# Kernel tuning notes

Measured on AMD Instinct MI355X. Metric: run time of the kernel, lower is better.

Reference implementation:

```python
import jax, jax.numpy as jnp
import numpy as np
from jax import lax

B, NBB, C, H, W = 32, 16, 1024, 22, 22
P = 3            # pooled output size (3x3)
SCALE = 1.0 / 16.0
EPS = 1e-5


def setup_inputs() -> dict:
    key = jax.random.key(0)
    ks = jax.random.split(key, 12)
    feat = jax.random.normal(ks[0], (B, C, H, W), jnp.float32)
    # bbox in xywh image coords, in-range for a 352x352 search region
    xy = jax.random.uniform(ks[1], (B, NBB, 2), jnp.float32, 0.0, 250.0)
    wh = jax.random.uniform(ks[2], (B, NBB, 2), jnp.float32, 16.0, 100.0)
    bbox = jnp.concatenate([xy, wh], axis=-1)
    conv_w = jax.random.normal(ks[3], (C, C, 3, 3), jnp.float32) * 0.01
    conv_b = jnp.zeros((C,), jnp.float32)
    bn_gamma = jnp.ones((C,), jnp.float32)
    bn_beta = jnp.zeros((C,), jnp.float32)
    bn_mean = jax.random.normal(ks[4], (C,), jnp.float32) * 0.1
    bn_var = jax.random.uniform(ks[5], (C,), jnp.float32, 0.5, 1.5)
    w1 = jax.random.normal(ks[6], (C // 2, C), jnp.float32) * 0.02
    b1 = jnp.zeros((C // 2,), jnp.float32)
    w2 = jax.random.normal(ks[7], (C // 2, C // 2), jnp.float32) * 0.02
    b2 = jnp.zeros((C // 2,), jnp.float32)
    w3 = jax.random.normal(ks[8], (512, C // 2), jnp.float32) * 0.02
    b3 = jnp.zeros((512,), jnp.float32)
    return dict(feat=feat, bbox=bbox, conv_w=conv_w, conv_b=conv_b,
                bn_gamma=bn_gamma, bn_beta=bn_beta, bn_mean=bn_mean, bn_var=bn_var,
                w1=w1, b1=b1, w2=w2, b2=b2, w3=w3, b3=b3)


def _hat_int(t):
    # Antiderivative of the bilinear hat h(u)=max(0,1-|u|), clipped to support.
    t = jnp.clip(t, -1.0, 1.0)
    return t + 0.5 - 0.5 * t * jnp.abs(t)


def _bin_weights(lo, bw, n):
    # lo, bw: [B, NBB].  Returns exact integral weights [B, NBB, P, n]:
    # W[b,r,p,i] = integral over bin p of hat(x - i) dx  (PrRoI closed form).
    p = jnp.arange(P, dtype=lo.dtype)
    xs = lo[..., None] + p * bw[..., None]          # [B,NBB,P] bin starts
    xe = xs + bw[..., None]                          # bin ends
    i = jnp.arange(n, dtype=lo.dtype)
    return _hat_int(xe[..., None] - i) - _hat_int(xs[..., None] - i)


def reference(feat, bbox, conv_w, conv_b, bn_gamma, bn_beta, bn_mean, bn_var,
              w1, b1, w2, b2, w3, b3):
    # --- PrRoI pooling (exact separable bilinear integral) ---
    x1 = bbox[..., 0] * SCALE
    y1 = bbox[..., 1] * SCALE
    x2 = (bbox[..., 0] + bbox[..., 2]) * SCALE
    y2 = (bbox[..., 1] + bbox[..., 3]) * SCALE
    bw = (x2 - x1) / P
    bh = (y2 - y1) / P
    Wx = _bin_weights(x1, bw, W)                     # [B,NBB,P,W]
    Wy = _bin_weights(y1, bh, H)                     # [B,NBB,P,H]
    pooled = jnp.einsum('bchw,bnqh,bnpw->bncqp', feat, Wy, Wx)  # [B,NBB,C,P,P]
    area = jnp.maximum(bw * bh, 0.0)[..., None, None, None]
    pooled = jnp.where(area > 0, pooled / jnp.maximum(area, 1e-12), 0.0)
    x = pooled.reshape(B * NBB, C, P, P)

    # --- conv_bn_relu: 3x3 conv, valid padding -> 1x1, BN (eval), ReLU ---
    x = lax.conv_general_dilated(x, conv_w, (1, 1), 'VALID',
                                 dimension_numbers=('NCHW', 'OIHW', 'NCHW'))
    x = x + conv_b[:, None, None]
    x = (x - bn_mean[:, None, None]) * (bn_gamma * lax.rsqrt(bn_var + EPS))[:, None, None]
    x = x + bn_beta[:, None, None]
    x = jax.nn.relu(x)

    # --- MLP head ---
    x = x.reshape(B * NBB, C)
    x = jax.nn.relu(x @ w1.T + b1)
    x = jax.nn.relu(x @ w2.T + b2)
    x = x @ w3.T + b3
    return x.reshape(B, NBB, 512)
```

## Files before the change

### kernel.cpp

```cpp
#include <hip/hip_runtime.h>
#include <hip/hip_bf16.h>

#define B_    32
#define NBB_  16
#define C_    1024
#define NROI  512
#define KCONV 9216
#define SCALE_ (1.0f/16.0f)
#define EPS_  1e-5f

using f32x4  = __attribute__((ext_vector_type(4))) float;
using bf16x8 = __attribute__((ext_vector_type(8))) short;

__device__ __forceinline__ unsigned f2bf(float f) {
  union { float f; unsigned u; } x; x.f = f;
  unsigned r = x.u + 0x7fffu + ((x.u >> 16) & 1u);
  return r >> 16;
}

__device__ __forceinline__ unsigned pk_bf16(float lo, float hi) {
  __hip_bfloat162 h = __float22bfloat162_rn(make_float2(lo, hi));
  return *reinterpret_cast<unsigned*>(&h);
}

__device__ __forceinline__ float hat_int(float t) {
  t = fminf(fmaxf(t, -1.f), 1.f);
  return t + 0.5f - 0.5f * t * fabsf(t);
}

__device__ __forceinline__ void glds16(const void* g, void* l) {
  __builtin_amdgcn_global_load_lds((const __attribute__((address_space(1))) void*)g,
                                   (__attribute__((address_space(3))) void*)l, 16, 0, 0);
}

__global__ __launch_bounds__(256) void prep_all(
    const float* __restrict__ bbox, const float* __restrict__ conv_w,
    const float* __restrict__ w1, const float* __restrict__ w2, const float* __restrict__ w3,
    unsigned short* __restrict__ W2d, unsigned short* __restrict__ Wfb,
    unsigned short* __restrict__ o1, unsigned short* __restrict__ o2,
    unsigned short* __restrict__ o3)
{
  __shared__ __align__(16) char psm[18504];
  int tid = threadIdx.x;
  int bx = blockIdx.x;

  if (bx < 32) {
    int b = bx;
    float* wyS = (float*)psm;
    float* wxS = wyS + 1056;
    for (int t = tid; t < 352; t += 256) {
      int n = t / 22, i = t - n * 22;
      float4 bb = ((const float4*)bbox)[b*16 + n];
      float x1 = bb.x * SCALE_, y1 = bb.y * SCALE_;
      float x2 = (bb.x + bb.z) * SCALE_, y2 = (bb.y + bb.w) * SCALE_;
      float bw = (x2 - x1) / 3.f, bh = (y2 - y1) / 3.f;
      float area = fmaxf(bw * bh, 0.f);
      float inv = area > 0.f ? 1.f / fmaxf(area, 1e-12f) : 0.f;
      float fi = (float)i;
#pragma unroll
      for (int q = 0; q < 3; ++q) {
        float sy = y1 + q * bh;
        wyS[n*66 + q*22 + i] = hat_int(sy + bh - fi) - hat_int(sy - fi);
        float sx = x1 + q * bw;
        wxS[n*66 + q*22 + i] = (hat_int(sx + bw - fi) - hat_int(sx - fi)) * inv;
      }
    }
    __syncthreads();
    if (tid < 144) {
      int n = tid / 9, qp = tid - n*9, q = qp / 3, p = qp - q*3;
      const float* wyp = wyS + n*66 + q*22;
      const float* wxp = wxS + n*66 + p*22;
      unsigned short* out = W2d + ((size_t)b*144 + tid) * 512;
      for (int h = 0; h < 22; ++h) {
        float yv = wyp[h];
        int kb = h * 22;
#pragma unroll
        for (int w = 0; w < 22; w += 2)
          *(unsigned*)&out[kb + w] = pk_bf16(yv * wxp[w], yv * wxp[w+1]);
      }
#pragma unroll
      for (int k = 484; k < 512; k += 2) *(unsigned*)&out[k] = 0u;
    }
  } else if (bx < 1056) {
    int o = bx - 32;
    unsigned short (*T)[1028] = (unsigned short(*)[1028])psm;
    const float4* src = (const float4*)(conv_w + (size_t)o * 9216);
#pragma unroll
    for (int it = 0; it < 9; ++it) {
      int i = tid + it * 256;
      float4 v = src[i];
      int e = i * 4;
      { int c = e / 9,     qp = e - c*9;             T[qp][c] = (unsigned short)f2bf(v.x); }
      { int ee = e+1; int c = ee / 9, qp = ee - c*9; T[qp][c] = (unsigned short)f2bf(v.y); }
      { int ee = e+2; int c = ee / 9, qp = ee - c*9; T[qp][c] = (unsigned short)f2bf(v.z); }
      { int ee = e+3; int c = ee / 9, qp = ee - c*9; T[qp][c] = (unsigned short)f2bf(v.w); }
    }
    __syncthreads();
    unsigned short* dst = Wfb + (size_t)o * 9216;
#pragma unroll
    for (int qp = 0; qp < 9; ++qp) {
      uint2 w = *(const uint2*)&T[qp][tid * 4];
      ((uint2*)(dst + qp * 1024))[tid] = w;
    }
  } else {
    int i = (bx - 1056) * 256 + tid;
    const float* src; unsigned short* dst; int g;
    if (i < 65536)      { src = w1; dst = o1; g = i; }
    else if (i < 98304) { src = w2; dst = o2; g = i - 65536; }
    else                { src = w3; dst = o3; g = i - 98304; }
    float4 a = ((const float4*)src)[2*g];
    float4 b = ((const float4*)src)[2*g + 1];
    uint4 pk;
    pk.x = pk_bf16(a.x, a.y); pk.y = pk_bf16(a.z, a.w);
    pk.z = pk_bf16(b.x, b.y); pk.w = pk_bf16(b.z, b.w);
    ((uint4*)dst)[g] = pk;
  }
}

__global__ __launch_bounds__(384) void pool_gemm(const float* __restrict__ feat,
                                                 const unsigned short* __restrict__ W2d,
                                                 unsigned short* __restrict__ X) {
  __shared__ __align__(16) unsigned short Bs[64 * 72];
  int tid = threadIdx.x;
  int nch = blockIdx.x, b = blockIdx.y;
  int lane = tid & 63, wid = tid >> 6;
  int wm = wid >> 1, wn = wid & 1;
  int l15 = lane & 15, kg = lane >> 4;
  const unsigned short* w2b = W2d + (size_t)b * 144 * 512;
  const float* fb = feat + ((size_t)b * C_ + (size_t)nch * 64) * 484;
  f32x4 acc[3][2] = {};

  int c0 = tid >> 4,        f40 = tid & 15;
  int i1 = tid + 384;  int c1 = i1 >> 4, f41 = i1 & 15;
  int i2 = tid + 768;  bool has2 = i2 < 1024; int c2 = i2 >> 4, f42 = i2 & 15;
  float4 bR0, bR1, bR2;

#define LOADB(s) do { \
    bR0 = (((s) < 7 || f40 <= 8) ? *(const float4*)(fb + (size_t)c0*484 + (s)*64 + f40*4) : make_float4(0,0,0,0)); \
    bR1 = (((s) < 7 || f41 <= 8) ? *(const float4*)(fb + (size_t)c1*484 + (s)*64 + f41*4) : make_float4(0,0,0,0)); \
    if (has2) bR2 = (((s) < 7 || f42 <= 8) ? *(const float4*)(fb + (size_t)c2*484 + (s)*64 + f42*4) : make_float4(0,0,0,0)); \
  } while (0)

  LOADB(0);
#pragma unroll
  for (int s = 0; s < 8; ++s) {
    __syncthreads();
    {
      uint2 p0; p0.x = pk_bf16(bR0.x, bR0.y); p0.y = pk_bf16(bR0.z, bR0.w);
      *(uint2*)&Bs[c0*72 + f40*4] = p0;
      uint2 p1; p1.x = pk_bf16(bR1.x, bR1.y); p1.y = pk_bf16(bR1.z, bR1.w);
      *(uint2*)&Bs[c1*72 + f41*4] = p1;
      if (has2) {
        uint2 p2; p2.x = pk_bf16(bR2.x, bR2.y); p2.y = pk_bf16(bR2.z, bR2.w);
        *(uint2*)&Bs[c2*72 + f42*4] = p2;
      }
    }
    if (s < 7) LOADB(s + 1);
    __syncthreads();

    bf16x8 af[3][2], bf[2][2];
#pragma unroll
    for (int fm = 0; fm < 3; ++fm)
#pragma unroll
      for (int kk = 0; kk < 2; ++kk)
        af[fm][kk] = *(const bf16x8*)(w2b + (size_t)(wm*48 + fm*16 + l15) * 512 + s*64 + kk*32 + kg*8);
#pragma unroll
    for (int fn = 0; fn < 2; ++fn)
#pragma unroll
      for (int kk = 0; kk < 2; ++kk)
        bf[fn][kk] = *(const bf16x8*)&Bs[(wn*32 + fn*16 + l15) * 72 + kk*32 + kg*8];
#pragma unroll
    for (int fm = 0; fm < 3; ++fm)
#pragma unroll
      for (int fn = 0; fn < 2; ++fn) {
        acc[fm][fn] = __builtin_amdgcn_mfma_f32_16x16x32_bf16(af[fm][0], bf[fn][0], acc[fm][fn], 0, 0, 0);
        acc[fm][fn] = __builtin_amdgcn_mfma_f32_16x16x32_bf16(af[fm][1], bf[fn][1], acc[fm][fn], 0, 0, 0);
      }
  }
#undef LOADB

#pragma unroll
  for (int fm = 0; fm < 3; ++fm)
#pragma unroll
    for (int r = 0; r < 4; ++r) {
      int m = wm*48 + fm*16 + kg*4 + r;
      int n = m / 9, qp = m - n*9;
      size_t base = ((size_t)(b*16 + n)) * KCONV + (size_t)qp * 1024 + (size_t)nch * 64;
#pragma unroll
      for (int fn = 0; fn < 2; ++fn)
        X[base + wn*32 + fn*16 + l15] = (unsigned short)f2bf(acc[fm][fn][r]);
    }
}

__global__ __launch_bounds__(256) void gemm128(const unsigned short* __restrict__ A,
                                               const unsigned short* __restrict__ Bm,
                                               float* __restrict__ Cp,
                                               int M, int N, int K, int kChunk) {
  __shared__ __align__(16) unsigned short As[2][4096];
  __shared__ __align__(16) unsigned short Bs[2][4096];
  int tid = threadIdx.x;
  int lane = tid & 63, wid = tid >> 6;
  int wm = wid >> 1, wn = wid & 1;
  int l15 = lane & 15, kg = lane >> 4;
  int nt = blockIdx.x, mt = blockIdx.y, z = blockIdx.z;
  int kbeg = z * kChunk;
  int steps = kChunk / 32;

  int row0 = tid >> 2, row1 = 64 + row0;
  int slot = tid & 3;
  int s0 = slot ^ ((row0 >> 1) & 3);
  int s1 = slot ^ ((row1 >> 1) & 3);
  const unsigned short* ga0 = A  + (size_t)(mt*128 + row0) * K + kbeg + s0*8;
  const unsigned short* ga1 = A  + (size_t)(mt*128 + row1) * K + kbeg + s1*8;
  const unsigned short* gb0 = Bm + (size_t)(nt*128 + row0) * K + kbeg + s0*8;
  const unsigned short* gb1 = Bm + (size_t)(nt*128 + row1) * K + kbeg + s1*8;
  int wbyte = wid * 1024;

  f32x4 acc[4][4] = {};
  int cur = 0;

#define ISSUE(buf, s) do { int ko = (s) * 32; \
    glds16(ga0 + ko, (char*)&As[(buf)][0] + wbyte); \
    glds16(ga1 + ko, (char*)&As[(buf)][0] + 4096 + wbyte); \
    glds16(gb0 + ko, (char*)&Bs[(buf)][0] + wbyte); \
    glds16(gb1 + ko, (char*)&Bs[(buf)][0] + 4096 + wbyte); } while (0)

  ISSUE(0, 0);
  for (int s = 0; s < steps; ++s) {
    __syncthreads();
    if (s + 1 < steps) ISSUE(cur ^ 1, s + 1);
    bf16x8 af[4], bfr[4];
#pragma unroll
    for (int fm = 0; fm < 4; ++fm) {
      int fr = wm*64 + fm*16 + l15;
      af[fm] = *(const bf16x8*)&As[cur][fr*32 + ((kg ^ ((fr >> 1) & 3)) << 3)];
    }
#pragma unroll
    for (int fn = 0; fn < 4; ++fn) {
      int fr = wn*64 + fn*16 + l15;
      bfr[fn] = *(const bf16x8*)&Bs[cur][fr*32 + ((kg ^ ((fr >> 1) & 3)) << 3)];
    }
#pragma unroll
    for (int fm = 0; fm < 4; ++fm)
#pragma unroll
      for (int fn = 0; fn < 4; ++fn)
        acc[fm][fn] = __builtin_amdgcn_mfma_f32_16x16x32_bf16(af[fm], bfr[fn], acc[fm][fn], 0, 0, 0);
    cur ^= 1;
  }
#undef ISSUE

  float* cp = Cp + ((size_t)z * M + (size_t)mt * 128) * N + (size_t)nt * 128;
#pragma unroll
  for (int fm = 0; fm < 4; ++fm)
#pragma unroll
    for (int fn = 0; fn < 4; ++fn)
#pragma unroll
      for (int r = 0; r < 4; ++r) {
        int row = wm*64 + fm*16 + kg*4 + r;
        int col = wn*64 + fn*16 + l15;
        cp[(size_t)row * N + col] = acc[fm][fn][r];
      }
}

__global__ __launch_bounds__(256) void epi0(const float* __restrict__ Cp, int SK, int MN4,
                                            const float* __restrict__ bias,
                                            const float* __restrict__ g,
                                            const float* __restrict__ be,
                                            const float* __restrict__ mu,
                                            const float* __restrict__ var,
                                            unsigned short* __restrict__ outb) {
  int i = blockIdx.x * 256 + threadIdx.x;
  if (i >= MN4) return;
  float4 s = ((const float4*)Cp)[i];
  for (int z = 1; z < SK; ++z) {
    float4 t = ((const float4*)Cp)[(size_t)z * MN4 + i];
    s.x += t.x; s.y += t.y; s.z += t.z; s.w += t.w;
  }
  int n0 = (i * 4) & 1023;
  float v[4] = {s.x, s.y, s.z, s.w};
  float o[4];
#pragma unroll
  for (int j = 0; j < 4; ++j) {
    int n = n0 + j;
    float sc = g[n] * rsqrtf(var[n] + EPS_);
    o[j] = fmaxf((v[j] + bias[n] - mu[n]) * sc + be[n], 0.f);
  }
  uint2 pk; pk.x = pk_bf16(o[0], o[1]); pk.y = pk_bf16(o[2], o[3]);
  *(uint2*)&outb[(size_t)i * 4] = pk;
}

template<int MODE>
__global__ __launch_bounds__(256) void gemm_full(const unsigned short* __restrict__ A,
                                                 const unsigned short* __restrict__ Bm,
                                                 int K,
                                                 const float* __restrict__ bias,
                                                 unsigned short* __restrict__ outb,
                                                 float* __restrict__ outf) {
  __shared__ __align__(16) unsigned short As[64][40];
  __shared__ __align__(16) unsigned short Bs[64][40];
  int tid = threadIdx.x;
  int lane = tid & 63, wid = tid >> 6;
  int wm = wid >> 1, wn = wid & 1;
  int l15 = lane & 15, kg = lane >> 4;
  int nt = blockIdx.x, mt = blockIdx.y;
  int srow = tid >> 2, sseg = tid & 3;
  const unsigned short* aG = A  + (size_t)(mt*64 + srow) * K + sseg * 8;
  const unsigned short* bG = Bm + (size_t)(nt*64 + srow) * K + sseg * 8;
  f32x4 acc[2][2] = {};

  for (int k0 = 0; k0 < K; k0 += 32) {
    uint4 av = *(const uint4*)(aG + k0);
    uint4 bv = *(const uint4*)(bG + k0);
    __syncthreads();
    *(uint4*)&As[srow][sseg*8] = av;
    *(uint4*)&Bs[srow][sseg*8] = bv;
    __syncthreads();
    bf16x8 a0 = *(const bf16x8*)&As[wm*32 +      l15][kg*8];
    bf16x8 a1 = *(const bf16x8*)&As[wm*32 + 16 + l15][kg*8];
    bf16x8 b0 = *(const bf16x8*)&Bs[wn*32 +      l15][kg*8];
    bf16x8 b1 = *(const bf16x8*)&Bs[wn*32 + 16 + l15][kg*8];
    acc[0][0] = __builtin_amdgcn_mfma_f32_16x16x32_bf16(a0, b0, acc[0][0], 0, 0, 0);
    acc[0][1] = __builtin_amdgcn_mfma_f32_16x16x32_bf16(a0, b1, acc[0][1], 0, 0, 0);
    acc[1][0] = __builtin_amdgcn_mfma_f32_16x16x32_bf16(a1, b0, acc[1][0], 0, 0, 0);
    acc[1][1] = __builtin_amdgcn_mfma_f32_16x16x32_bf16(a1, b1, acc[1][1], 0, 0, 0);
  }

#pragma unroll
  for (int fm = 0; fm < 2; ++fm)
#pragma unroll
    for (int fn = 0; fn < 2; ++fn)
#pragma unroll
      for (int r = 0; r < 4; ++r) {
        int grow = mt*64 + wm*32 + fm*16 + kg*4 + r;
        int gcol = nt*64 + wn*32 + fn*16 + l15;
        float v = acc[fm][fn][r] + bias[gcol];
        if (MODE == 1)
          outb[(size_t)grow * 512 + gcol] = (unsigned short)f2bf(fmaxf(v, 0.f));
        else
          outf[(size_t)grow * 512 + gcol] = v;
      }
}

extern "C" void kernel_launch(void* const* d_in, const int* in_sizes, int n_in,
                              void* d_out, int out_size, void* d_ws, size_t ws_size,
                              hipStream_t stream) {
  const float* feat   = (const float*)d_in[0];
  const float* bbox   = (const float*)d_in[1];
  const float* conv_w = (const float*)d_in[2];
  const float* conv_b = (const float*)d_in[3];
  const float* gamma  = (const float*)d_in[4];
  const float* beta   = (const float*)d_in[5];
  const float* mean   = (const float*)d_in[6];
  const float* var    = (const float*)d_in[7];
  const float* w1     = (const float*)d_in[8];
  const float* b1     = (const float*)d_in[9];
  const float* w2     = (const float*)d_in[10];
  const float* b2     = (const float*)d_in[11];
  const float* w3     = (const float*)d_in[12];
  const float* b3     = (const float*)d_in[13];

  char* ws = (char*)d_ws;
  unsigned short* W2d = (unsigned short*)(ws);
  unsigned short* Xb  = (unsigned short*)(ws + 4718592);
  unsigned short* Wfb = (unsigned short*)(ws + 14155776);
  unsigned short* w1b = (unsigned short*)(ws + 33030144);
  unsigned short* w2b = (unsigned short*)(ws + 34078720);
  unsigned short* w3b = (unsigned short*)(ws + 34603008);
  float*          part= (float*)(ws + 35127296);
  unsigned short* H0  = (unsigned short*)(ws + 51904512);
  unsigned short* H1  = (unsigned short*)(ws + 52953088);
  unsigned short* H2  = (unsigned short*)(ws + 53477376);

  prep_all<<<1568, 256, 0, stream>>>(bbox, conv_w, w1, w2, w3, W2d, Wfb, w1b, w2b, w3b);

  pool_gemm<<<dim3(16, 32), 384, 0, stream>>>(feat, W2d, Xb);

  gemm128<<<dim3(8, 4, 8), 256, 0, stream>>>(Xb, Wfb, part, 512, 1024, 9216, 1152);
  epi0<<<512, 256, 0, stream>>>(part, 8, 131072, conv_b, gamma, beta, mean, var, H0);

  gemm_full<1><<<dim3(8, 8), 256, 0, stream>>>(H0, w1b, 1024, b1, H1, nullptr);
  gemm_full<1><<<dim3(8, 8), 256, 0, stream>>>(H1, w2b, 512,  b2, H2, nullptr);
  gemm_full<2><<<dim3(8, 8), 256, 0, stream>>>(H2, w3b, 512,  b3, nullptr, (float*)d_out);
}
```

Measured before the change: 124.4 us.

## Use native c*9+qp K-order to drop conv weight transpose, stage X through LDS

The conv weight conversion no longer transposes each output channel through shared memory into a qp-major K layout. It becomes a flat, fully coalesced fp32-to-bf16 pack over many more blocks. To keep the GEMM consistent, pool_gemm now writes its activations in the matching channel-major (c*9+qp) K order, staging the tile in LDS and then emitting contiguous 32-bit stores instead of scattered 16-bit stores. This adds an extra LDS buffer and a barrier in pool_gemm, and the prep launch grows to thousands of small blocks.

Result: no change. 123.1 us (-1.1%).

```diff
diff --git a/kernel.cpp b/kernel.cpp
--- a/kernel.cpp
+++ b/kernel.cpp
@@ -40,14 +40,24 @@
     unsigned short* __restrict__ o1, unsigned short* __restrict__ o2,
     unsigned short* __restrict__ o3)
 {
-  __shared__ __align__(16) char psm[18504];
+  __shared__ __align__(16) float psm[2112];
   int tid = threadIdx.x;
   int bx = blockIdx.x;
 
+  if (bx >= 32 && bx < 4640) {
+    int g = (bx - 32) * 256 + tid;
+    float4 a = ((const float4*)conv_w)[2*g];
+    float4 b = ((const float4*)conv_w)[2*g + 1];
+    uint4 pk;
+    pk.x = pk_bf16(a.x, a.y); pk.y = pk_bf16(a.z, a.w);
+    pk.z = pk_bf16(b.x, b.y); pk.w = pk_bf16(b.z, b.w);
+    ((uint4*)Wfb)[g] = pk;
+    return;
+  }
   if (bx < 32) {
     int b = bx;
-    float* wyS = (float*)psm;
-    float* wxS = wyS + 1056;
+    float* wyS = psm;
+    float* wxS = psm + 1056;
     for (int t = tid; t < 352; t += 256) {
       int n = t / 22, i = t - n * 22;
       float4 bb = ((const float4*)bbox)[b*16 + n];
@@ -81,29 +91,8 @@
 #pragma unroll
       for (int k = 484; k < 512; k += 2) *(unsigned*)&out[k] = 0u;
     }
-  } else if (bx < 1056) {
-    int o = bx - 32;
-    unsigned short (*T)[1028] = (unsigned short(*)[1028])psm;
-    const float4* src = (const float4*)(conv_w + (size_t)o * 9216);
-#pragma unroll
-    for (int it = 0; it < 9; ++it) {
-      int i = tid + it * 256;
-      float4 v = src[i];
-      int e = i * 4;
-      { int c = e / 9,     qp = e - c*9;             T[qp][c] = (unsigned short)f2bf(v.x); }
-      { int ee = e+1; int c = ee / 9, qp = ee - c*9; T[qp][c] = (unsigned short)f2bf(v.y); }
-      { int ee = e+2; int c = ee / 9, qp = ee - c*9; T[qp][c] = (unsigned short)f2bf(v.z); }
-      { int ee = e+3; int c = ee / 9, qp = ee - c*9; T[qp][c] = (unsigned short)f2bf(v.w); }
-    }
-    __syncthreads();
-    unsigned short* dst = Wfb + (size_t)o * 9216;
-#pragma unroll
-    for (int qp = 0; qp < 9; ++qp) {
-      uint2 w = *(const uint2*)&T[qp][tid * 4];
-      ((uint2*)(dst + qp * 1024))[tid] = w;
-    }
   } else {
-    int i = (bx - 1056) * 256 + tid;
+    int i = (bx - 4640) * 256 + tid;
     const float* src; unsigned short* dst; int g;
     if (i < 65536)      { src = w1; dst = o1; g = i; }
     else if (i < 98304) { src = w2; dst = o2; g = i - 65536; }
@@ -121,6 +110,7 @@
                                                  const unsigned short* __restrict__ W2d,
                                                  unsigned short* __restrict__ X) {
   __shared__ __align__(16) unsigned short Bs[64 * 72];
+  __shared__ __align__(16) unsigned short Xs[16][580];
   int tid = threadIdx.x;
   int nch = blockIdx.x, b = blockIdx.y;
   int lane = tid & 63, wid = tid >> 6;
@@ -185,11 +175,18 @@
     for (int r = 0; r < 4; ++r) {
       int m = wm*48 + fm*16 + kg*4 + r;
       int n = m / 9, qp = m - n*9;
-      size_t base = ((size_t)(b*16 + n)) * KCONV + (size_t)qp * 1024 + (size_t)nch * 64;
-#pragma unroll
-      for (int fn = 0; fn < 2; ++fn)
-        X[base + wn*32 + fn*16 + l15] = (unsigned short)f2bf(acc[fm][fn][r]);
-    }
+#pragma unroll
+      for (int fn = 0; fn < 2; ++fn) {
+        int c = wn*32 + fn*16 + l15;
+        Xs[n][c*9 + qp] = (unsigned short)f2bf(acc[fm][fn][r]);
+      }
+    }
+  __syncthreads();
+  for (int idx = tid; idx < 4608; idx += 384) {
+    int n = idx / 288, j = idx - n * 288;
+    *(unsigned*)&X[((size_t)(b*16 + n)) * KCONV + (size_t)nch * 576 + j*2] =
+        *(const unsigned*)&Xs[n][j*2];
+  }
 }
 
 __global__ __launch_bounds__(256) void gemm128(const unsigned short* __restrict__ A,
@@ -371,7 +368,7 @@
   unsigned short* H1  = (unsigned short*)(ws + 52953088);
   unsigned short* H2  = (unsigned short*)(ws + 53477376);
 
-  prep_all<<<1568, 256, 0, stream>>>(bbox, conv_w, w1, w2, w3, W2d, Wfb, w1b, w2b, w3b);
+  prep_all<<<5152, 256, 0, stream>>>(bbox, conv_w, w1, w2, w3, W2d, Wfb, w1b, w2b, w3b);
 
   pool_gemm<<<dim3(16, 32), 384, 0, stream>>>(feat, W2d, Xb);
 
```
